# Kernel tuning notes

Measured on AMD Instinct MI355X. Metric: run time of the kernel, lower is better.

The kernel has to match this reference:

```python
import jax, jax.numpy as jnp
import numpy as np

TAU = 1.0  # temperature of the tanh-Gumbel relaxation


def setup_inputs() -> dict:
    key = jax.random.key(0)
    k1, k2, k3 = jax.random.split(key, 3)
    B, C, F, W, H, K, S = 64, 256, 512, 64, 64, 3, 1
    x = jax.random.normal(k1, (B, C, W, H), dtype=jnp.float32)
    weight = jax.random.normal(k2, (F, C, K, K), dtype=jnp.float32) * 0.05
    # torch samples Uniform(1e-10, 1) fresh every forward; we make it an input
    epsilon = jax.random.uniform(k3, (S, F, C, K, K), dtype=jnp.float32,
                                 minval=1e-10, maxval=1.0)
    return {"x": x, "weight": weight, "epsilon": epsilon}


def reference(x, weight, epsilon):
    # delta: logistic noise; relaxed_weights = tanh((w + delta)/tau)
    delta = 0.5 * jnp.log(epsilon / (1.0 - epsilon))          # [s,f,c,k,l]
    relaxed_weights = jnp.tanh((weight + delta) / TAU)        # broadcast over s
    x5 = x[None]                                              # [1,b,c,w,h]
    # sums over kernel dims k,l (independent of x) and contracts channel c
    out = jnp.einsum('sfckl,sbcwh->sbfwh', relaxed_weights, x5)
    return out
```

## Files before the change

kernel.cpp:

```cpp
#include <hip/hip_runtime.h>
#include <hip/hip_bf16.h>
#include <stdint.h>

#define C_DIM 256
#define F_DIM 512
#define B_DIM 64
#define N_DIM 4096
#define BN 128
#define BF 128
#define BK 64
#define NSTEP 16

typedef __bf16  bf16x8 __attribute__((ext_vector_type(8)));
typedef float   f32x4  __attribute__((ext_vector_type(4)));

__global__ void prep_w2(const float* __restrict__ w, const float* __restrict__ eps,
                        __hip_bfloat16* __restrict__ w2) {
    int id = blockIdx.x * blockDim.x + threadIdx.x;
    if (id >= F_DIM * C_DIM) return;
    const float* wp = w  + id * 9;
    const float* ep = eps + id * 9;
    float s = 0.f;
#pragma unroll
    for (int i = 0; i < 9; ++i) {
        float wi = wp[i], e = ep[i];
        float r = e / (1.0f - e);
        float t = __expf(2.0f * wi) * r;
        s += 1.0f - 2.0f / (t + 1.0f);
    }
    w2[id] = __float2bfloat16(s);
}

__device__ inline void load_lds16(const void* g, void* l) {
    __builtin_amdgcn_global_load_lds(
        (const __attribute__((address_space(1))) uint32_t*)g,
        (__attribute__((address_space(3))) uint32_t*)l, 16, 0, 0);
}

__device__ inline uint32_t pack_bf16x2(float a, float b) {
    union { __hip_bfloat162 h; uint32_t u; } c;
    c.h.x = __float2bfloat16(a);
    c.h.y = __float2bfloat16(b);
    return c.u;
}

__global__ __launch_bounds__(512, 4)
void gemm_kernel(const float* __restrict__ X,
                 const __hip_bfloat16* __restrict__ W2,
                 float* __restrict__ Out) {
    __shared__ unsigned char sX[BN * 512];
    __shared__ unsigned char sA[BF * BK * 2];

    const int tid  = threadIdx.x;
    const int lane = tid & 63;
    const int wave = tid >> 6;
    const int l15  = lane & 15;
    const int l4   = lane >> 4;

    const int bi = blockIdx.x >> 5;
    const int ni = blockIdx.x & 31;

    const float* Xb = X   + (size_t)bi * C_DIM * N_DIM + ni * BN;
    float*       Ob = Out + (size_t)bi * F_DIM * N_DIM + ni * BN;

    {
        const int n  = tid & 127;
        const int ch = tid >> 7;
        unsigned char* base = sX + n * 512;
        const int sw = (n & 31) << 4;
        const float* xp = Xb + n;
#pragma unroll
        for (int g = 0; g < 8; ++g) {
            const int c0 = ch * 64 + g * 8;
            float v[8];
#pragma unroll
            for (int r = 0; r < 8; ++r)
                v[r] = __builtin_nontemporal_load(xp + (size_t)(c0 + r) * N_DIM);
            uint4 pk;
            pk.x = pack_bf16x2(v[0], v[1]);
            pk.y = pack_bf16x2(v[2], v[3]);
            pk.z = pack_bf16x2(v[4], v[5]);
            pk.w = pack_bf16x2(v[6], v[7]);
            *(uint4*)(base + ((c0 * 2) ^ sw)) = pk;
        }
    }

    const int wm = (wave >> 1) * 32;
    const int wn = (wave & 1) * 64;

    f32x4 acc[2][4];
#pragma unroll
    for (int mi = 0; mi < 2; ++mi)
#pragma unroll
        for (int nj = 0; nj < 4; ++nj)
            acc[mi][nj] = (f32x4){0.f, 0.f, 0.f, 0.f};

    for (int step = 0; step < NSTEP; ++step) {
        const int ft = step >> 2;
        const int kt = (step & 3) * BK;

        __syncthreads();

        {
            const __hip_bfloat16* Aft = W2 + (size_t)ft * BF * C_DIM + kt;
#pragma unroll
            for (int j = 0; j < 2; ++j) {
                int s = j * 512 + tid;
                int m = s >> 3, g = s & 7;
                const __hip_bfloat16* gp = Aft + m * C_DIM + ((g ^ (m & 7)) * 8);
                char* lp = (char*)sA + (j * 512 + wave * 64) * 16;
                load_lds16((const void*)gp, (void*)lp);
            }
        }

        __syncthreads();

        bf16x8 af[2][2], bfr[2][4];
#pragma unroll
        for (int kk = 0; kk < 2; ++kk) {
#pragma unroll
            for (int mi = 0; mi < 2; ++mi) {
                int m   = wm + mi * 16 + l15;
                int col = (kk * 64 + l4 * 16) ^ ((m & 7) << 4);
                af[kk][mi] = *(const bf16x8*)(sA + m * 128 + col);
            }
#pragma unroll
            for (int nj = 0; nj < 4; ++nj) {
                int n   = wn + nj * 16 + l15;
                int col = (kt * 2 + kk * 64 + l4 * 16) ^ ((n & 31) << 4);
                bfr[kk][nj] = *(const bf16x8*)(sX + n * 512 + col);
            }
        }
#pragma unroll
        for (int kk = 0; kk < 2; ++kk)
#pragma unroll
            for (int mi = 0; mi < 2; ++mi)
#pragma unroll
                for (int nj = 0; nj < 4; ++nj)
                    acc[mi][nj] = __builtin_amdgcn_mfma_f32_16x16x32_bf16(
                        af[kk][mi], bfr[kk][nj], acc[mi][nj], 0, 0, 0);

        if ((step & 3) == 3) {
            float* Oft = Ob + (size_t)(ft * BF) * N_DIM;
#pragma unroll
            for (int mi = 0; mi < 2; ++mi) {
                int mrow = wm + mi * 16 + l4 * 4;
#pragma unroll
                for (int nj = 0; nj < 4; ++nj) {
                    int ncol = wn + nj * 16 + l15;
                    float* op = Oft + (size_t)mrow * N_DIM + ncol;
#pragma unroll
                    for (int r = 0; r < 4; ++r)
                        __builtin_nontemporal_store(acc[mi][nj][r], op + (size_t)r * N_DIM);
                    acc[mi][nj] = (f32x4){0.f, 0.f, 0.f, 0.f};
                }
            }
        }
    }
}

extern "C" void kernel_launch(void* const* d_in, const int* in_sizes, int n_in,
                              void* d_out, int out_size, void* d_ws, size_t ws_size,
                              hipStream_t stream) {
    const float* x   = (const float*)d_in[0];
    const float* w   = (const float*)d_in[1];
    const float* eps = (const float*)d_in[2];
    float* out       = (float*)d_out;
    __hip_bfloat16* w2 = (__hip_bfloat16*)d_ws;

    prep_w2<<<dim3((F_DIM * C_DIM + 255) / 256), dim3(256), 0, stream>>>(w, eps, w2);
    gemm_kernel<<<dim3(B_DIM * 32), dim3(512), 0, stream>>>(x, w2, out);
}
```

Baseline: 745.7 us.

## Read weights directly from global and overlap X staging with first MMAs

Drops the LDS staging of the small bf16 weight tile. Each wave now loads its A fragments straight from global/L2, which removes two barriers per k-step. X is loaded in two halves: the first 128 channels are packed into LDS, and the MMAs on that half run while the loads for the upper 128 channels are still in flight. The restructured loop unrolls the K dimension fully per F tile. The cost is more global load traffic for weights, since each wave reloads them, plus higher register pressure from holding 32 floats of X across the first compute phase.

```diff
diff --git a/kernel.cpp b/kernel.cpp
--- a/kernel.cpp
+++ b/kernel.cpp
@@ -8,8 +8,6 @@
 #define N_DIM 4096
 #define BN 128
 #define BF 128
-#define BK 64
-#define NSTEP 16
 
 typedef __bf16  bf16x8 __attribute__((ext_vector_type(8)));
 typedef float   f32x4  __attribute__((ext_vector_type(4)));
@@ -31,12 +29,6 @@
     w2[id] = __float2bfloat16(s);
 }
 
-__device__ inline void load_lds16(const void* g, void* l) {
-    __builtin_amdgcn_global_load_lds(
-        (const __attribute__((address_space(1))) uint32_t*)g,
-        (__attribute__((address_space(3))) uint32_t*)l, 16, 0, 0);
-}
-
 __device__ inline uint32_t pack_bf16x2(float a, float b) {
     union { __hip_bfloat162 h; uint32_t u; } c;
     c.h.x = __float2bfloat16(a);
@@ -49,7 +41,6 @@
                  const __hip_bfloat16* __restrict__ W2,
                  float* __restrict__ Out) {
     __shared__ unsigned char sX[BN * 512];
-    __shared__ unsigned char sA[BF * BK * 2];
 
     const int tid  = threadIdx.x;
     const int lane = tid & 63;
@@ -63,27 +54,41 @@
     const float* Xb = X   + (size_t)bi * C_DIM * N_DIM + ni * BN;
     float*       Ob = Out + (size_t)bi * F_DIM * N_DIM + ni * BN;
 
-    {
-        const int n  = tid & 127;
-        const int ch = tid >> 7;
-        unsigned char* base = sX + n * 512;
-        const int sw = (n & 31) << 4;
-        const float* xp = Xb + n;
+    const int sn = tid & 127;
+    const int sc = (tid >> 7) * 32;
+    unsigned char* sbase = sX + sn * 512;
+    const int sw = (sn & 31) << 4;
+    const float* xp = Xb + sn;
+
+    float vlo[4][8];
 #pragma unroll
-        for (int g = 0; g < 8; ++g) {
-            const int c0 = ch * 64 + g * 8;
-            float v[8];
+    for (int g = 0; g < 4; ++g) {
+        const int c0 = sc + g * 8;
 #pragma unroll
-            for (int r = 0; r < 8; ++r)
-                v[r] = __builtin_nontemporal_load(xp + (size_t)(c0 + r) * N_DIM);
-            uint4 pk;
-            pk.x = pack_bf16x2(v[0], v[1]);
-            pk.y = pack_bf16x2(v[2], v[3]);
-            pk.z = pack_bf16x2(v[4], v[5]);
-            pk.w = pack_bf16x2(v[6], v[7]);
-            *(uint4*)(base + ((c0 * 2) ^ sw)) = pk;
-        }
+        for (int r = 0; r < 8; ++r)
+            vlo[g][r] = __builtin_nontemporal_load(xp + (size_t)(c0 + r) * N_DIM);
     }
+#pragma unroll
+    for (int g = 0; g < 4; ++g) {
+        const int c0 = sc + g * 8;
+        uint4 pk;
+        pk.x = pack_bf16x2(vlo[g][0], vlo[g][1]);
+        pk.y = pack_bf16x2(vlo[g][2], vlo[g][3]);
+        pk.z = pack_bf16x2(vlo[g][4], vlo[g][5]);
+        pk.w = pack_bf16x2(vlo[g][6], vlo[g][7]);
+        *(uint4*)(sbase + ((c0 * 2) ^ sw)) = pk;
+    }
+
+    float vhi[4][8];
+#pragma unroll
+    for (int g = 0; g < 4; ++g) {
+        const int c0 = 128 + sc + g * 8;
+#pragma unroll
+        for (int r = 0; r < 8; ++r)
+            vhi[g][r] = __builtin_nontemporal_load(xp + (size_t)(c0 + r) * N_DIM);
+    }
+
+    __syncthreads();
 
     const int wm = (wave >> 1) * 32;
     const int wn = (wave & 1) * 64;
@@ -95,67 +100,66 @@
         for (int nj = 0; nj < 4; ++nj)
             acc[mi][nj] = (f32x4){0.f, 0.f, 0.f, 0.f};
 
-    for (int step = 0; step < NSTEP; ++step) {
-        const int ft = step >> 2;
-        const int kt = (step & 3) * BK;
+    auto step = [&](const __hip_bfloat16* Aw, int kq) {
+        bf16x8 a0 = *(const bf16x8*)(Aw + kq * 32);
+        bf16x8 a1 = *(const bf16x8*)(Aw + 16 * C_DIM + kq * 32);
+        bf16x8 b[4];
+#pragma unroll
+        for (int nj = 0; nj < 4; ++nj) {
+            const int nn  = wn + nj * 16 + l15;
+            const int col = (kq * 64 + l4 * 16) ^ ((nn & 31) << 4);
+            b[nj] = *(const bf16x8*)(sX + nn * 512 + col);
+        }
+#pragma unroll
+        for (int nj = 0; nj < 4; ++nj) {
+            acc[0][nj] = __builtin_amdgcn_mfma_f32_16x16x32_bf16(a0, b[nj], acc[0][nj], 0, 0, 0);
+            acc[1][nj] = __builtin_amdgcn_mfma_f32_16x16x32_bf16(a1, b[nj], acc[1][nj], 0, 0, 0);
+        }
+    };
 
-        __syncthreads();
-
-        {
-            const __hip_bfloat16* Aft = W2 + (size_t)ft * BF * C_DIM + kt;
+    auto epilogue = [&](int ft) {
+        float* Oft = Ob + (size_t)(ft * BF) * N_DIM;
 #pragma unroll
-            for (int j = 0; j < 2; ++j) {
-                int s = j * 512 + tid;
-                int m = s >> 3, g = s & 7;
-                const __hip_bfloat16* gp = Aft + m * C_DIM + ((g ^ (m & 7)) * 8);
-                char* lp = (char*)sA + (j * 512 + wave * 64) * 16;
-                load_lds16((const void*)gp, (void*)lp);
+        for (int mi = 0; mi < 2; ++mi) {
+            const int mrow = wm + mi * 16 + l4 * 4;
+#pragma unroll
+            for (int nj = 0; nj < 4; ++nj) {
+                const int ncol = wn + nj * 16 + l15;
+                float* op = Oft + (size_t)mrow * N_DIM + ncol;
+#pragma unroll
+                for (int r = 0; r < 4; ++r)
+                    __builtin_nontemporal_store(acc[mi][nj][r], op + (size_t)r * N_DIM);
+                acc[mi][nj] = (f32x4){0.f, 0.f, 0.f, 0.f};
             }
         }
+    };
 
-        __syncthreads();
+    const __hip_bfloat16* AwBase = W2 + (size_t)(wm + l15) * C_DIM + l4 * 8;
 
-        bf16x8 af[2][2], bfr[2][4];
 #pragma unroll
-        for (int kk = 0; kk < 2; ++kk) {
+    for (int kq = 0; kq < 4; ++kq) step(AwBase, kq);
+
 #pragma unroll
-            for (int mi = 0; mi < 2; ++mi) {
-                int m   = wm + mi * 16 + l15;
-                int col = (kk * 64 + l4 * 16) ^ ((m & 7) << 4);
-                af[kk][mi] = *(const bf16x8*)(sA + m * 128 + col);
-            }
+    for (int g = 0; g < 4; ++g) {
+        const int c0 = 128 + sc + g * 8;
+        uint4 pk;
+        pk.x = pack_bf16x2(vhi[g][0], vhi[g][1]);
+        pk.y = pack_bf16x2(vhi[g][2], vhi[g][3]);
+        pk.z = pack_bf16x2(vhi[g][4], vhi[g][5]);
+        pk.w = pack_bf16x2(vhi[g][6], vhi[g][7]);
+        *(uint4*)(sbase + ((c0 * 2) ^ sw)) = pk;
+    }
+    __syncthreads();
+
 #pragma unroll
-            for (int nj = 0; nj < 4; ++nj) {
-                int n   = wn + nj * 16 + l15;
-                int col = (kt * 2 + kk * 64 + l4 * 16) ^ ((n & 31) << 4);
-                bfr[kk][nj] = *(const bf16x8*)(sX + n * 512 + col);
-            }
-        }
+    for (int kq = 4; kq < 8; ++kq) step(AwBase, kq);
+    epilogue(0);
+
+    for (int ft = 1; ft < 4; ++ft) {
+        const __hip_bfloat16* Aw = AwBase + (size_t)ft * BF * C_DIM;
 #pragma unroll
-        for (int kk = 0; kk < 2; ++kk)
-#pragma unroll
-            for (int mi = 0; mi < 2; ++mi)
-#pragma unroll
-                for (int nj = 0; nj < 4; ++nj)
-                    acc[mi][nj] = __builtin_amdgcn_mfma_f32_16x16x32_bf16(
-                        af[kk][mi], bfr[kk][nj], acc[mi][nj], 0, 0, 0);
-
-        if ((step & 3) == 3) {
-            float* Oft = Ob + (size_t)(ft * BF) * N_DIM;
-#pragma unroll
-            for (int mi = 0; mi < 2; ++mi) {
-                int mrow = wm + mi * 16 + l4 * 4;
-#pragma unroll
-                for (int nj = 0; nj < 4; ++nj) {
-                    int ncol = wn + nj * 16 + l15;
-                    float* op = Oft + (size_t)mrow * N_DIM + ncol;
-#pragma unroll
-                    for (int r = 0; r < 4; ++r)
-                        __builtin_nontemporal_store(acc[mi][nj][r], op + (size_t)r * N_DIM);
-                    acc[mi][nj] = (f32x4){0.f, 0.f, 0.f, 0.f};
-                }
-            }
-        }
+        for (int kq = 0; kq < 8; ++kq) step(Aw, kq);
+        epilogue(ft);
     }
 }
 
```

Result: slower. 783.7 us (+5.1%).
